# Kernel optimization log

Measured on AMD Instinct MI355X. Metric: run time of the kernel, lower is better.

Reference implementation:

```python
import jax, jax.numpy as jnp
import numpy as np
import math

B, S, D, H, NF = 2, 2048, 1024, 16, 4
DH = D // H


def setup_inputs() -> dict:
    key = jax.random.key(0)
    ks = jax.random.split(key, 8)
    scale = 0.01 / math.sqrt(D)  # rough attenuated-kaiming scale for projections
    return {
        "x": jax.random.normal(ks[0], (B, S, D), dtype=jnp.float32),
        "weights": jax.random.uniform(ks[1], (1, NF), dtype=jnp.float32),
        "Wq": jax.random.normal(ks[2], (D, D), dtype=jnp.float32) * scale,
        "bq": jnp.zeros((D,), dtype=jnp.float32),
        "Wk": jax.random.normal(ks[3], (D, D), dtype=jnp.float32) * scale,
        "bk": jnp.zeros((D,), dtype=jnp.float32),
        "Wv": jax.random.normal(ks[4], (D, D), dtype=jnp.float32) * scale,
        "bv": jnp.zeros((D,), dtype=jnp.float32),
        "Wout": jax.random.normal(ks[5], (NF, D, D), dtype=jnp.float32) / math.sqrt(D),
        "bout": jnp.zeros((NF, D), dtype=jnp.float32),
    }


def reference(x, weights, Wq, bq, Wk, bk, Wv, bv, Wout, bout):
    # projections (torch Linear: x @ W.T + b)
    q = x @ Wq.T + bq  # [B,S,D]
    k = x @ Wk.T + bk
    v = x @ Wv.T + bv
    # split heads -> [B,H,S,DH]
    split = lambda t: t.reshape(B, S, H, DH).transpose(0, 2, 1, 3)
    q, k, v = split(q), split(k), split(v)
    # scores with causal additive mask of -10000 (as in get_attention_mask)
    scores = jnp.einsum("bhqd,bhkd->bhqk", q, k) / math.sqrt(DH)
    i = jnp.arange(S)
    causal = (i[None, :] <= i[:, None])  # [S,S] True where allowed
    mask = (1.0 - causal.astype(scores.dtype)) * -10000.0
    attn = jax.nn.softmax(scores + mask, axis=-1)
    # dropout is disabled (p=0.0)
    out = jnp.einsum("bhqk,bhkd->bhqd", attn, v)  # [B,H,S,DH]
    out = out.transpose(0, 2, 1, 3).reshape(B, S, D)
    # WeightedFunctions: per-function Linear(d,d) combined by weights[0]
    w0 = weights[0]  # [NF]
    Weff = jnp.einsum("f,fod->od", w0, Wout)  # [D,D]
    beff = w0 @ bout  # [D]
    return out @ Weff.T + beff
```

## Files before the change

### kernel.cpp

```cpp
#include <hip/hip_runtime.h>


typedef unsigned short u16;
typedef __bf16 bf16_t;
typedef bf16_t bf16x8 __attribute__((ext_vector_type(8)));
typedef bf16_t bf16x4 __attribute__((ext_vector_type(4)));
typedef float f32x4 __attribute__((ext_vector_type(4)));
typedef u16 u16x8 __attribute__((ext_vector_type(8)));
typedef u16 u16x4 __attribute__((ext_vector_type(4)));

#define DEV __device__ __forceinline__

DEV u16 f2bf(float f) {
  unsigned u = __float_as_uint(f);
  u += 0x7FFFu + ((u >> 16) & 1u);
  return (u16)(u >> 16);
}

DEV void async_ld16(const void* g, void* lds_wave_uniform) {
  __builtin_amdgcn_global_load_lds(
      (const __attribute__((address_space(1))) void*)g,
      (__attribute__((address_space(3))) void*)lds_wave_uniform, 16, 0, 0);
}

__global__ __launch_bounds__(256) void cvt_bf16_kernel(
    const float* __restrict__ in, u16* __restrict__ out, int n4) {
  int i = blockIdx.x * blockDim.x + threadIdx.x;
  const int stride = gridDim.x * blockDim.x;
  for (; i < n4; i += stride) {
    const float4 v = ((const float4*)in)[i];
    u16x4 o;
    o[0] = f2bf(v.x); o[1] = f2bf(v.y); o[2] = f2bf(v.z); o[3] = f2bf(v.w);
    ((u16x4*)out)[i] = o;
  }
}

__global__ __launch_bounds__(256) void cvt3_bf16_kernel(
    const float* __restrict__ a, const float* __restrict__ b,
    const float* __restrict__ c, u16* __restrict__ out) {
  const int i = blockIdx.x * 256 + threadIdx.x;
  const int which = i >> 18;
  const int j = i & 262143;
  const float* src = which == 0 ? a : (which == 1 ? b : c);
  const float4 v = ((const float4*)src)[j];
  u16x4 o;
  o[0] = f2bf(v.x); o[1] = f2bf(v.y); o[2] = f2bf(v.z); o[3] = f2bf(v.w);
  ((u16x4*)out)[i] = o;
}

__global__ __launch_bounds__(256) void build_weff_kernel(
    const float* __restrict__ w4, const float* __restrict__ Wout,
    const float* __restrict__ bout, u16* __restrict__ Weff,
    float* __restrict__ beff) {
  constexpr int DD4 = 262144;
  const int i = blockIdx.x * blockDim.x + threadIdx.x;
  if (i >= DD4) return;
  const float w0 = w4[0], w1 = w4[1], w2 = w4[2], w3 = w4[3];
  const float4* W = (const float4*)Wout;
  const float4 a = W[i], b1 = W[DD4 + i], b2 = W[2 * DD4 + i], b3 = W[3 * DD4 + i];
  u16x4 o;
  o[0] = f2bf(w0 * a.x + w1 * b1.x + w2 * b2.x + w3 * b3.x);
  o[1] = f2bf(w0 * a.y + w1 * b1.y + w2 * b2.y + w3 * b3.y);
  o[2] = f2bf(w0 * a.z + w1 * b1.z + w2 * b2.z + w3 * b3.z);
  o[3] = f2bf(w0 * a.w + w1 * b1.w + w2 * b2.w + w3 * b3.w);
  ((u16x4*)Weff)[i] = o;
  if (i < 256) {
    const float4* B4 = (const float4*)bout;
    const float4 ba = B4[i], c1 = B4[256 + i], c2 = B4[512 + i], c3 = B4[768 + i];
    float4 ob;
    ob.x = w0 * ba.x + w1 * c1.x + w2 * c2.x + w3 * c3.x;
    ob.y = w0 * ba.y + w1 * c1.y + w2 * c2.y + w3 * c3.y;
    ob.z = w0 * ba.z + w1 * c1.z + w2 * c2.z + w3 * c3.z;
    ob.w = w0 * ba.w + w1 * c1.w + w2 * c2.w + w3 * c3.w;
    ((float4*)beff)[i] = ob;
  }
}

__global__ __launch_bounds__(256) void gemm_bt_kernel(
    const u16* __restrict__ A, const u16* __restrict__ Bw,
    const float* __restrict__ bias, float* __restrict__ C, int M, int N, int K) {
  constexpr int BM = 128, BK = 32;
  __shared__ u16 As[2][BM * BK];
  __shared__ u16 Bs[2][BM * BK];
  const int tid = threadIdx.x;
  const int w = tid >> 6, lane = tid & 63;
  const int l15 = lane & 15, l4 = lane >> 4;
  const int wr = w >> 1, wc = w & 1;
  const long m0 = (long)blockIdx.y * BM, n0 = (long)blockIdx.x * BM;

  const int sr = (tid * 16) >> 6;
  const int sc = ((tid * 16) & 63) >> 1;

  auto stage = [&](int buf, int kt) {
#pragma unroll
    for (int is = 0; is < 2; ++is) {
      const int r = sr + is * 64;
      async_ld16(A + (m0 + r) * K + kt + sc, &As[buf][w * 512 + is * 2048]);
      async_ld16(Bw + (n0 + r) * K + kt + sc, &Bs[buf][w * 512 + is * 2048]);
    }
  };

  f32x4 acc[4][4] = {};
  stage(0, 0);
  __syncthreads();
  const int nt = K / BK;
  for (int t = 0; t < nt; ++t) {
    const int buf = t & 1;
    if (t + 1 < nt) stage(buf ^ 1, (t + 1) * BK);
    bf16x8 af[4], bfrag[4];
#pragma unroll
    for (int i = 0; i < 4; ++i) {
      af[i] = *(const bf16x8*)&As[buf][(wr * 64 + i * 16 + l15) * BK + l4 * 8];
      bfrag[i] = *(const bf16x8*)&Bs[buf][(wc * 64 + i * 16 + l15) * BK + l4 * 8];
    }
#pragma unroll
    for (int i = 0; i < 4; ++i)
#pragma unroll
      for (int j = 0; j < 4; ++j)
        acc[i][j] = __builtin_amdgcn_mfma_f32_16x16x32_bf16(af[i], bfrag[j],
                                                            acc[i][j], 0, 0, 0);
    __syncthreads();
  }

#pragma unroll
  for (int i = 0; i < 4; ++i) {
    const long row0 = m0 + wr * 64 + i * 16 + l4 * 4;
#pragma unroll
    for (int j = 0; j < 4; ++j) {
      const long col = n0 + wc * 64 + j * 16 + l15;
      const float bb = bias[col];
#pragma unroll
      for (int r = 0; r < 4; ++r)
        C[(row0 + r) * N + col] = acc[i][j][r] + bb;
    }
  }
}

__global__ __launch_bounds__(256) void gemm_qkv_kernel(
    const u16* __restrict__ A, const u16* __restrict__ Bw,
    const float* __restrict__ bq, const float* __restrict__ bk,
    const float* __restrict__ bv, u16* __restrict__ qo, u16* __restrict__ ko,
    u16* __restrict__ vo) {
  constexpr int K = 1024, BK = 32;
  __shared__ u16 SM[16384];
  u16* As = SM;
  u16* Bs = SM + 8192;
  const int tid = threadIdx.x;
  const int w = tid >> 6, lane = tid & 63;
  const int l15 = lane & 15, l4 = lane >> 4;
  const int wr = w >> 1, wc = w & 1;
  const long m0 = (long)blockIdx.y * 128, n0 = (long)blockIdx.x * 128;
  const int seg = blockIdx.x >> 3;
  const float* bias = seg == 0 ? bq : (seg == 1 ? bk : bv);
  u16* outp = seg == 0 ? qo : (seg == 1 ? ko : vo);
  const float scale = seg == 0 ? 0.18033688011112042f : 1.0f;

  const int sr = (tid * 16) >> 6;
  const int sc = ((tid * 16) & 63) >> 1;

  auto stage = [&](int buf, int kt) {
#pragma unroll
    for (int is = 0; is < 2; ++is) {
      const int r = sr + is * 64;
      async_ld16(A + (m0 + r) * K + kt + sc, &As[buf * 4096 + w * 512 + is * 2048]);
      async_ld16(Bw + (n0 + r) * K + kt + sc, &Bs[buf * 4096 + w * 512 + is * 2048]);
    }
  };

  f32x4 acc[4][4] = {};
  stage(0, 0);
  __syncthreads();
  const int nt = K / BK;
  for (int t = 0; t < nt; ++t) {
    const int buf = t & 1;
    if (t + 1 < nt) stage(buf ^ 1, (t + 1) * BK);
    bf16x8 af[4], bfrag[4];
#pragma unroll
    for (int i = 0; i < 4; ++i) {
      af[i] = *(const bf16x8*)&As[buf * 4096 + (wr * 64 + i * 16 + l15) * BK + l4 * 8];
      bfrag[i] = *(const bf16x8*)&Bs[buf * 4096 + (wc * 64 + i * 16 + l15) * BK + l4 * 8];
    }
#pragma unroll
    for (int i = 0; i < 4; ++i)
#pragma unroll
      for (int j = 0; j < 4; ++j)
        acc[i][j] = __builtin_amdgcn_mfma_f32_16x16x32_bf16(af[i], bfrag[j],
                                                            acc[i][j], 0, 0, 0);
    __syncthreads();
  }

  const long ccol0 = n0 - (long)seg * 1024;
#pragma unroll
  for (int i = 0; i < 4; ++i) {
#pragma unroll
    for (int j = 0; j < 4; ++j) {
      const int colb = wc * 64 + j * 16 + l15;
      const float bb = bias[ccol0 + colb];
#pragma unroll
      for (int r = 0; r < 4; ++r) {
        const int row = wr * 64 + i * 16 + l4 * 4 + r;
        SM[row * 128 + (colb ^ ((row & 15) << 3))] =
            f2bf((acc[i][j][r] + bb) * scale);
      }
    }
  }
  __syncthreads();
#pragma unroll
  for (int p = 0; p < 8; ++p) {
    const int cid = p * 256 + tid;
    const int row = cid >> 4, c = cid & 15;
    const u16x8 vch = *(const u16x8*)&SM[row * 128 + ((c ^ (row & 15)) * 8)];
    *(u16x8*)&outp[(m0 + row) * 1024 + ccol0 + c * 8] = vch;
  }
}

__global__ __launch_bounds__(256) void transpose_v_kernel(
    const u16* __restrict__ V, u16* __restrict__ Vt) {
  constexpr int S = 2048, D = 1024, DH = 64;
  __shared__ u16 T[64 * 72];
  const int tid = threadIdx.x;
  const int bh = blockIdx.y, b = bh >> 4, h = bh & 15;
  const int s0 = blockIdx.x * 64;
#pragma unroll
  for (int is = 0; is < 2; ++is) {
    const int sl = tid + is * 256;
    const int r = sl >> 3, c0 = (sl & 7) * 8;
    *(u16x8*)&T[r * 72 + c0] =
        *(const u16x8*)(V + (size_t)(b * S + s0 + r) * D + h * DH + c0);
  }
  __syncthreads();
#pragma unroll
  for (int is = 0; is < 2; ++is) {
    const int sl = tid + is * 256;
    const int d = sl >> 3, k0 = (sl & 7) * 8;
    u16x8 o;
#pragma unroll
    for (int j = 0; j < 8; ++j) o[j] = T[(k0 + j) * 72 + d];
    *(u16x8*)(Vt + (size_t)(bh * DH + d) * S + s0 + k0) = o;
  }
}

__global__ __launch_bounds__(512, 6) void flash_kernel(
    const u16* __restrict__ Q, const u16* __restrict__ Kg,
    const u16* __restrict__ Vt, u16* __restrict__ O,
    u16* __restrict__ accP, float* __restrict__ mP, float* __restrict__ lP) {
  constexpr int S = 2048, D = 1024, DH = 64;
  __shared__ u16 Ks[2][4096];
  __shared__ u16 Vs[2][4096];
  __shared__ u16 Ps[8192];
  const int tid = threadIdx.x;
  const int w = tid >> 6, lane = tid & 63;
  const int l15 = lane & 15, l4 = lane >> 4;
  const int bh = blockIdx.y, b = bh >> 4, h = bh & 15;
  const int x = 23 - (int)blockIdx.x;
  int bi, kvlo, kvhi, seg;
  if (x < 8) {
    bi = x; seg = -1; kvlo = 0; kvhi = 2 * bi + 2;
  } else {
    const int idx = x - 8;
    bi = 8 + (idx >> 1); seg = idx & 1;
    kvlo = seg ? (bi + 1) : 0;
    kvhi = seg ? (2 * bi + 2) : (bi + 1);
  }
  const int qw = 128 * bi + w * 16;
  const int qtile = qw >> 6;

  const u16* Kbh = Kg + (size_t)b * S * D + h * DH;
  const u16* Vbh = Vt + (size_t)bh * DH * S;

  const int srow = tid >> 3;
  const int scol = ((tid & 7) ^ (srow & 7)) * 8;
  const int sw = l15 & 7;

  bf16x8 qf[2];
  {
    const u16* qp = Q + (size_t)(b * S + qw + l15) * D + h * DH + l4 * 8;
    qf[0] = *(const bf16x8*)qp;
    qf[1] = *(const bf16x8*)(qp + 32);
  }

  f32x4 acc_o[4] = {};
  float m_run = -3e38f, l_run = 0.f;

  async_ld16(Kbh + (size_t)(kvlo * 64 + srow) * D + scol, &Ks[0][w * 512]);
  async_ld16(Vbh + (size_t)srow * S + kvlo * 64 + scol, &Vs[0][w * 512]);
  __syncthreads();

  for (int it = kvlo; it < kvhi; ++it) {
    const int buf = (it - kvlo) & 1;
    if (it + 1 < kvhi) {
      async_ld16(Kbh + (size_t)((it + 1) * 64 + srow) * D + scol,
                 &Ks[buf ^ 1][w * 512]);
      async_ld16(Vbh + (size_t)srow * S + (it + 1) * 64 + scol,
                 &Vs[buf ^ 1][w * 512]);
    }
    if (it <= qtile) {
      f32x4 accs[4] = {};
#pragma unroll
      for (int cb = 0; cb < 4; ++cb) {
        const int row = cb * 16 + l15;
        const bf16x8 kf0 = *(const bf16x8*)&Ks[buf][row * 64 + ((l4 ^ sw) * 8)];
        const bf16x8 kf1 =
            *(const bf16x8*)&Ks[buf][row * 64 + (((l4 + 4) ^ sw) * 8)];
        accs[cb] =
            __builtin_amdgcn_mfma_f32_16x16x32_bf16(kf0, qf[0], accs[cb], 0, 0, 0);
        accs[cb] =
            __builtin_amdgcn_mfma_f32_16x16x32_bf16(kf1, qf[1], accs[cb], 0, 0, 0);
      }
      float mx = -3e38f;
      if (it == qtile) {
#pragma unroll
        for (int cb = 0; cb < 4; ++cb)
#pragma unroll
          for (int r = 0; r < 4; ++r) {
            float s_ = accs[cb][r];
            if (it * 64 + cb * 16 + l4 * 4 + r > qw + l15) s_ = -3e38f;
            accs[cb][r] = s_;
            mx = fmaxf(mx, s_);
          }
      } else {
#pragma unroll
        for (int cb = 0; cb < 4; ++cb)
#pragma unroll
          for (int r = 0; r < 4; ++r) mx = fmaxf(mx, accs[cb][r]);
      }
      mx = fmaxf(mx, __shfl_xor(mx, 16));
      mx = fmaxf(mx, __shfl_xor(mx, 32));
      if (!__all(mx - m_run <= 8.0f)) {
        const float mn = fmaxf(m_run, mx);
        const float corr = __builtin_amdgcn_exp2f(m_run - mn);
        m_run = mn;
        float cq[4];
#pragma unroll
        for (int r = 0; r < 4; ++r) cq[r] = __shfl(corr, l4 * 4 + r, 64);
#pragma unroll
        for (int db = 0; db < 4; ++db)
#pragma unroll
          for (int r = 0; r < 4; ++r) acc_o[db][r] *= cq[r];
        l_run *= corr;
      }
      float rs = 0.f;
#pragma unroll
      for (int cb = 0; cb < 4; ++cb)
#pragma unroll
        for (int r = 0; r < 4; ++r) {
          const float pv = __builtin_amdgcn_exp2f(accs[cb][r] - m_run);
          accs[cb][r] = pv;
          rs += pv;
        }
      rs += __shfl_xor(rs, 16);
      rs += __shfl_xor(rs, 32);
      l_run += rs;
#pragma unroll
      for (int cb = 0; cb < 4; ++cb) {
        bf16x4 pk = {(bf16_t)accs[cb][0], (bf16_t)accs[cb][1],
                     (bf16_t)accs[cb][2], (bf16_t)accs[cb][3]};
        const int chunk = (2 * cb + (l4 >> 1)) ^ sw;
        *(bf16x4*)&Ps[w * 1024 + l15 * 64 + chunk * 8 + (l4 & 1) * 4] = pk;
      }
      asm volatile("s_waitcnt lgkmcnt(0)" ::: "memory");
      bf16x8 pa[2];
#pragma unroll
      for (int mf = 0; mf < 2; ++mf) {
        const int chunk = (mf * 4 + l4) ^ sw;
        pa[mf] = *(const bf16x8*)&Ps[w * 1024 + l15 * 64 + chunk * 8];
      }
#pragma unroll
      for (int db = 0; db < 4; ++db) {
        const int row = db * 16 + l15;
        const bf16x8 vf0 = *(const bf16x8*)&Vs[buf][row * 64 + ((l4 ^ sw) * 8)];
        const bf16x8 vf1 =
            *(const bf16x8*)&Vs[buf][row * 64 + (((l4 + 4) ^ sw) * 8)];
        acc_o[db] =
            __builtin_amdgcn_mfma_f32_16x16x32_bf16(pa[0], vf0, acc_o[db], 0, 0, 0);
        acc_o[db] =
            __builtin_amdgcn_mfma_f32_16x16x32_bf16(pa[1], vf1, acc_o[db], 0, 0, 0);
      }
    }
    __syncthreads();
  }

  float lq[4];
  if (seg < 0) {
#pragma unroll
    for (int r = 0; r < 4; ++r) lq[r] = __shfl(l_run, l4 * 4 + r, 64);
  }
#pragma unroll
  for (int db = 0; db < 4; ++db) {
#pragma unroll
    for (int r = 0; r < 4; ++r) {
      const int row = l4 * 4 + r;
      const int col = db * 16 + l15;
      const float v = seg < 0 ? acc_o[db][r] / lq[r] : acc_o[db][r];
      Ps[w * 1024 + row * 64 + (col ^ ((row & 7) << 3))] = f2bf(v);
    }
  }
  asm volatile("s_waitcnt lgkmcnt(0)" ::: "memory");
  if (seg < 0) {
#pragma unroll
    for (int j = 0; j < 2; ++j) {
      const int cid = j * 64 + lane;
      const int row = cid >> 3, c = cid & 7;
      const u16x8 vch =
          *(const u16x8*)&Ps[w * 1024 + row * 64 + ((c ^ (row & 7)) * 8)];
      *(u16x8*)&O[(size_t)(b * S + qw + row) * D + h * DH + c * 8] = vch;
    }
  } else {
    const size_t base = (size_t)seg * 32768 + (size_t)bh * 1024 + (qw - 1024);
#pragma unroll
    for (int j = 0; j < 2; ++j) {
      const int cid = j * 64 + lane;
      const int row = cid >> 3, c = cid & 7;
      const u16x8 vch =
          *(const u16x8*)&Ps[w * 1024 + row * 64 + ((c ^ (row & 7)) * 8)];
      *(u16x8*)&accP[(base + row) * 64 + c * 8] = vch;
    }
    if (l4 == 0) {
      mP[base + l15] = m_run;
      lP[base + l15] = l_run;
    }
  }
}

__global__ __launch_bounds__(256) void combine_kernel(
    const u16* __restrict__ accP, const float* __restrict__ mP,
    const float* __restrict__ lP, u16* __restrict__ O) {
  const int id = blockIdx.x * 256 + threadIdx.x;
  const int row = id >> 3;
  const int c0 = (id & 7) * 8;
  const float m0 = mP[row], m1 = mP[32768 + row];
  const float l0 = lP[row], l1 = lP[32768 + row];
  const float M = fmaxf(m0, m1);
  const float e0 = __builtin_amdgcn_exp2f(m0 - M);
  const float e1 = __builtin_amdgcn_exp2f(m1 - M);
  const float inv = 1.f / (l0 * e0 + l1 * e1);
  const bf16_t* aP = (const bf16_t*)accP;
  const bf16x8 a0 = *(const bf16x8*)&aP[(size_t)row * 64 + c0];
  const bf16x8 a1 = *(const bf16x8*)&aP[(size_t)(32768 + row) * 64 + c0];
  const int bh = row >> 10, s = 1024 + (row & 1023);
  const int b = bh >> 4, h = bh & 15;
  bf16_t* out = (bf16_t*)O + (size_t)(b * 2048 + s) * 1024 + h * 64 + c0;
  bf16x8 o;
#pragma unroll
  for (int j = 0; j < 8; ++j)
    o[j] = (bf16_t)(((float)a0[j] * e0 + (float)a1[j] * e1) * inv);
  *(bf16x8*)out = o;
}

extern "C" void kernel_launch(void* const* d_in, const int* in_sizes, int n_in,
                              void* d_out, int out_size, void* d_ws, size_t ws_size,
                              hipStream_t stream) {
  (void)in_sizes; (void)n_in; (void)out_size;
  const float* x   = (const float*)d_in[0];
  const float* wts = (const float*)d_in[1];
  const float* Wq  = (const float*)d_in[2];
  const float* bq  = (const float*)d_in[3];
  const float* Wk  = (const float*)d_in[4];
  const float* bk  = (const float*)d_in[5];
  const float* Wv  = (const float*)d_in[6];
  const float* bv  = (const float*)d_in[7];
  const float* Wo  = (const float*)d_in[8];
  const float* bo  = (const float*)d_in[9];
  float* out = (float*)d_out;

  if (ws_size < 58724352) return;

  char* ws = (char*)d_ws;
  u16* xbf  = (u16*)(ws + 0);
  u16* qbf  = (u16*)(ws + 8388608);
  u16* kbf  = (u16*)(ws + 16777216);
  u16* vbf  = (u16*)(ws + 25165824);
  u16* vt   = (u16*)(ws + 33554432);
  u16* attn = (u16*)(ws + 41943040);
  u16* wqkv = (u16*)(ws + 50331648);
  u16* wob  = (u16*)(ws + 56623104);
  float* beff = (float*)(ws + 58720256);

  u16* accP = xbf;
  float* mP = (float*)(ws + 50331648);
  float* lP = mP + 65536;

  cvt_bf16_kernel<<<2048, 256, 0, stream>>>(x, xbf, 1048576);
  cvt3_bf16_kernel<<<3072, 256, 0, stream>>>(Wq, Wk, Wv, wqkv);
  build_weff_kernel<<<1024, 256, 0, stream>>>(wts, Wo, bo, wob, beff);

  gemm_qkv_kernel<<<dim3(24, 32), 256, 0, stream>>>(xbf, wqkv, bq, bk, bv,
                                                    qbf, kbf, vbf);
  transpose_v_kernel<<<dim3(32, 32), 256, 0, stream>>>(vbf, vt);
  flash_kernel<<<dim3(24, 32), 512, 0, stream>>>(qbf, kbf, vt, attn,
                                                 accP, mP, lP);
  combine_kernel<<<1024, 256, 0, stream>>>(accP, mP, lP, attn);
  gemm_bt_kernel<<<dim3(8, 32), 256, 0, stream>>>(
      attn, wob, beff, out, 4096, 1024, 1024);
}
```

Before: 126.7 us.

## Fuse prep kernels, widen GEMM K-tile with swizzle, fuse V transpose, defer row reductions

Merges the three conversion and weight-combine kernels into one grid-stride prep kernel. Both GEMMs now use a 64-wide K tile with an XOR-swizzled LDS layout and two MFMAs per fragment pair. The QKV GEMM writes V already transposed through LDS, which removes the separate transpose kernel and the round trip of V through global memory. In the flash kernel, the cross-lane max and sum shuffles are skipped on the fast path, and the row-sum reduction happens once at the end. The cost is larger LDS use per block, which may reduce occupancy.

```diff
diff --git a/kernel.cpp b/kernel.cpp
--- a/kernel.cpp
+++ b/kernel.cpp
@@ -23,102 +23,113 @@
       (__attribute__((address_space(3))) void*)lds_wave_uniform, 16, 0, 0);
 }
 
-__global__ __launch_bounds__(256) void cvt_bf16_kernel(
-    const float* __restrict__ in, u16* __restrict__ out, int n4) {
-  int i = blockIdx.x * blockDim.x + threadIdx.x;
-  const int stride = gridDim.x * blockDim.x;
-  for (; i < n4; i += stride) {
-    const float4 v = ((const float4*)in)[i];
-    u16x4 o;
-    o[0] = f2bf(v.x); o[1] = f2bf(v.y); o[2] = f2bf(v.z); o[3] = f2bf(v.w);
-    ((u16x4*)out)[i] = o;
-  }
-}
-
-__global__ __launch_bounds__(256) void cvt3_bf16_kernel(
-    const float* __restrict__ a, const float* __restrict__ b,
-    const float* __restrict__ c, u16* __restrict__ out) {
-  const int i = blockIdx.x * 256 + threadIdx.x;
-  const int which = i >> 18;
-  const int j = i & 262143;
-  const float* src = which == 0 ? a : (which == 1 ? b : c);
-  const float4 v = ((const float4*)src)[j];
-  u16x4 o;
-  o[0] = f2bf(v.x); o[1] = f2bf(v.y); o[2] = f2bf(v.z); o[3] = f2bf(v.w);
-  ((u16x4*)out)[i] = o;
-}
-
-__global__ __launch_bounds__(256) void build_weff_kernel(
+__global__ __launch_bounds__(256) void prep_kernel(
+    const float* __restrict__ x, const float* __restrict__ Wq,
+    const float* __restrict__ Wk, const float* __restrict__ Wv,
     const float* __restrict__ w4, const float* __restrict__ Wout,
-    const float* __restrict__ bout, u16* __restrict__ Weff,
-    float* __restrict__ beff) {
-  constexpr int DD4 = 262144;
-  const int i = blockIdx.x * blockDim.x + threadIdx.x;
-  if (i >= DD4) return;
-  const float w0 = w4[0], w1 = w4[1], w2 = w4[2], w3 = w4[3];
-  const float4* W = (const float4*)Wout;
-  const float4 a = W[i], b1 = W[DD4 + i], b2 = W[2 * DD4 + i], b3 = W[3 * DD4 + i];
-  u16x4 o;
-  o[0] = f2bf(w0 * a.x + w1 * b1.x + w2 * b2.x + w3 * b3.x);
-  o[1] = f2bf(w0 * a.y + w1 * b1.y + w2 * b2.y + w3 * b3.y);
-  o[2] = f2bf(w0 * a.z + w1 * b1.z + w2 * b2.z + w3 * b3.z);
-  o[3] = f2bf(w0 * a.w + w1 * b1.w + w2 * b2.w + w3 * b3.w);
-  ((u16x4*)Weff)[i] = o;
-  if (i < 256) {
-    const float4* B4 = (const float4*)bout;
-    const float4 ba = B4[i], c1 = B4[256 + i], c2 = B4[512 + i], c3 = B4[768 + i];
-    float4 ob;
-    ob.x = w0 * ba.x + w1 * c1.x + w2 * c2.x + w3 * c3.x;
-    ob.y = w0 * ba.y + w1 * c1.y + w2 * c2.y + w3 * c3.y;
-    ob.z = w0 * ba.z + w1 * c1.z + w2 * c2.z + w3 * c3.z;
-    ob.w = w0 * ba.w + w1 * c1.w + w2 * c2.w + w3 * c3.w;
-    ((float4*)beff)[i] = ob;
-  }
-}
+    const float* __restrict__ bout, u16* __restrict__ xbf,
+    u16* __restrict__ wqkv, u16* __restrict__ Weff, float* __restrict__ beff) {
+  constexpr int NX = 1048576;
+  constexpr int NW = 262144;
+  const int stride = gridDim.x * 256;
+  for (int id = blockIdx.x * 256 + threadIdx.x; id < NX + 3 * NW + NW;
+       id += stride) {
+    if (id < NX) {
+      const float4 v = ((const float4*)x)[id];
+      u16x4 o;
+      o[0] = f2bf(v.x); o[1] = f2bf(v.y); o[2] = f2bf(v.z); o[3] = f2bf(v.w);
+      ((u16x4*)xbf)[id] = o;
+    } else if (id < NX + 3 * NW) {
+      const int wi = id - NX;
+      const int which = wi >> 18, j = wi & (NW - 1);
+      const float* src = which == 0 ? Wq : (which == 1 ? Wk : Wv);
+      const float4 v = ((const float4*)src)[j];
+      u16x4 o;
+      o[0] = f2bf(v.x); o[1] = f2bf(v.y); o[2] = f2bf(v.z); o[3] = f2bf(v.w);
+      ((u16x4*)wqkv)[wi] = o;
+    } else {
+      const int i = id - NX - 3 * NW;
+      const float w0 = w4[0], w1 = w4[1], w2 = w4[2], w3 = w4[3];
+      const float4* W = (const float4*)Wout;
+      const float4 a = W[i], b1 = W[NW + i], b2 = W[2 * NW + i],
+                   b3 = W[3 * NW + i];
+      u16x4 o;
+      o[0] = f2bf(w0 * a.x + w1 * b1.x + w2 * b2.x + w3 * b3.x);
+      o[1] = f2bf(w0 * a.y + w1 * b1.y + w2 * b2.y + w3 * b3.y);
+      o[2] = f2bf(w0 * a.z + w1 * b1.z + w2 * b2.z + w3 * b3.z);
+      o[3] = f2bf(w0 * a.w + w1 * b1.w + w2 * b2.w + w3 * b3.w);
+      ((u16x4*)Weff)[i] = o;
+      if (i < 256) {
+        const float4* B4 = (const float4*)bout;
+        const float4 ba = B4[i], c1 = B4[256 + i], c2 = B4[512 + i],
+                     c3 = B4[768 + i];
+        float4 ob;
+        ob.x = w0 * ba.x + w1 * c1.x + w2 * c2.x + w3 * c3.x;
+        ob.y = w0 * ba.y + w1 * c1.y + w2 * c2.y + w3 * c3.y;
+        ob.z = w0 * ba.z + w1 * c1.z + w2 * c2.z + w3 * c3.z;
+        ob.w = w0 * ba.w + w1 * c1.w + w2 * c2.w + w3 * c3.w;
+        ((float4*)beff)[i] = ob;
+      }
+    }
+  }
+}
+
 
 __global__ __launch_bounds__(256) void gemm_bt_kernel(
     const u16* __restrict__ A, const u16* __restrict__ Bw,
     const float* __restrict__ bias, float* __restrict__ C, int M, int N, int K) {
-  constexpr int BM = 128, BK = 32;
-  __shared__ u16 As[2][BM * BK];
-  __shared__ u16 Bs[2][BM * BK];
+  __shared__ u16 LDS[32768];
   const int tid = threadIdx.x;
   const int w = tid >> 6, lane = tid & 63;
   const int l15 = lane & 15, l4 = lane >> 4;
   const int wr = w >> 1, wc = w & 1;
-  const long m0 = (long)blockIdx.y * BM, n0 = (long)blockIdx.x * BM;
-
-  const int sr = (tid * 16) >> 6;
-  const int sc = ((tid * 16) & 63) >> 1;
-
+  const long m0 = (long)blockIdx.y * 128, n0 = (long)blockIdx.x * 128;
+
+  int srow[4], scol[4];
+#pragma unroll
+  for (int d = 0; d < 4; ++d) {
+    srow[d] = d * 32 + w * 8 + (lane >> 3);
+    scol[d] = ((lane & 7) ^ (srow[d] & 7)) * 8;
+  }
   auto stage = [&](int buf, int kt) {
 #pragma unroll
-    for (int is = 0; is < 2; ++is) {
-      const int r = sr + is * 64;
-      async_ld16(A + (m0 + r) * K + kt + sc, &As[buf][w * 512 + is * 2048]);
-      async_ld16(Bw + (n0 + r) * K + kt + sc, &Bs[buf][w * 512 + is * 2048]);
+    for (int d = 0; d < 4; ++d) {
+      async_ld16(A + (m0 + srow[d]) * K + kt + scol[d],
+                 &LDS[buf * 8192 + d * 2048 + w * 512]);
+      async_ld16(Bw + (n0 + srow[d]) * K + kt + scol[d],
+                 &LDS[16384 + buf * 8192 + d * 2048 + w * 512]);
     }
   };
 
   f32x4 acc[4][4] = {};
   stage(0, 0);
   __syncthreads();
-  const int nt = K / BK;
+  const int nt = K / 64;
   for (int t = 0; t < nt; ++t) {
     const int buf = t & 1;
-    if (t + 1 < nt) stage(buf ^ 1, (t + 1) * BK);
-    bf16x8 af[4], bfrag[4];
+    if (t + 1 < nt) stage(buf ^ 1, (t + 1) * 64);
+    bf16x8 af[4][2], bf[4][2];
 #pragma unroll
     for (int i = 0; i < 4; ++i) {
-      af[i] = *(const bf16x8*)&As[buf][(wr * 64 + i * 16 + l15) * BK + l4 * 8];
-      bfrag[i] = *(const bf16x8*)&Bs[buf][(wc * 64 + i * 16 + l15) * BK + l4 * 8];
+      const int ra = wr * 64 + i * 16 + l15;
+      const int rb = wc * 64 + i * 16 + l15;
+#pragma unroll
+      for (int ks = 0; ks < 2; ++ks) {
+        af[i][ks] = *(const bf16x8*)&LDS[buf * 8192 + ra * 64 +
+                                         (((ks * 4 + l4) ^ (ra & 7)) * 8)];
+        bf[i][ks] = *(const bf16x8*)&LDS[16384 + buf * 8192 + rb * 64 +
+                                         (((ks * 4 + l4) ^ (rb & 7)) * 8)];
+      }
     }
 #pragma unroll
     for (int i = 0; i < 4; ++i)
 #pragma unroll
-      for (int j = 0; j < 4; ++j)
-        acc[i][j] = __builtin_amdgcn_mfma_f32_16x16x32_bf16(af[i], bfrag[j],
+      for (int j = 0; j < 4; ++j) {
+        acc[i][j] = __builtin_amdgcn_mfma_f32_16x16x32_bf16(af[i][0], bf[j][0],
                                                             acc[i][j], 0, 0, 0);
+        acc[i][j] = __builtin_amdgcn_mfma_f32_16x16x32_bf16(af[i][1], bf[j][1],
+                                                            acc[i][j], 0, 0, 0);
+      }
     __syncthreads();
   }
 
@@ -140,11 +151,9 @@
     const u16* __restrict__ A, const u16* __restrict__ Bw,
     const float* __restrict__ bq, const float* __restrict__ bk,
     const float* __restrict__ bv, u16* __restrict__ qo, u16* __restrict__ ko,
-    u16* __restrict__ vo) {
-  constexpr int K = 1024, BK = 32;
-  __shared__ u16 SM[16384];
-  u16* As = SM;
-  u16* Bs = SM + 8192;
+    u16* __restrict__ vt) {
+  constexpr int K = 1024;
+  __shared__ u16 LDS[32768];
   const int tid = threadIdx.x;
   const int w = tid >> 6, lane = tid & 63;
   const int l15 = lane & 15, l4 = lane >> 4;
@@ -152,91 +161,107 @@
   const long m0 = (long)blockIdx.y * 128, n0 = (long)blockIdx.x * 128;
   const int seg = blockIdx.x >> 3;
   const float* bias = seg == 0 ? bq : (seg == 1 ? bk : bv);
-  u16* outp = seg == 0 ? qo : (seg == 1 ? ko : vo);
   const float scale = seg == 0 ? 0.18033688011112042f : 1.0f;
 
-  const int sr = (tid * 16) >> 6;
-  const int sc = ((tid * 16) & 63) >> 1;
-
+  int srow[4], scol[4];
+#pragma unroll
+  for (int d = 0; d < 4; ++d) {
+    srow[d] = d * 32 + w * 8 + (lane >> 3);
+    scol[d] = ((lane & 7) ^ (srow[d] & 7)) * 8;
+  }
   auto stage = [&](int buf, int kt) {
 #pragma unroll
-    for (int is = 0; is < 2; ++is) {
-      const int r = sr + is * 64;
-      async_ld16(A + (m0 + r) * K + kt + sc, &As[buf * 4096 + w * 512 + is * 2048]);
-      async_ld16(Bw + (n0 + r) * K + kt + sc, &Bs[buf * 4096 + w * 512 + is * 2048]);
+    for (int d = 0; d < 4; ++d) {
+      async_ld16(A + (m0 + srow[d]) * K + kt + scol[d],
+                 &LDS[buf * 8192 + d * 2048 + w * 512]);
+      async_ld16(Bw + (n0 + srow[d]) * K + kt + scol[d],
+                 &LDS[16384 + buf * 8192 + d * 2048 + w * 512]);
     }
   };
 
   f32x4 acc[4][4] = {};
   stage(0, 0);
   __syncthreads();
-  const int nt = K / BK;
+  const int nt = K / 64;
   for (int t = 0; t < nt; ++t) {
     const int buf = t & 1;
-    if (t + 1 < nt) stage(buf ^ 1, (t + 1) * BK);
-    bf16x8 af[4], bfrag[4];
+    if (t + 1 < nt) stage(buf ^ 1, (t + 1) * 64);
+    bf16x8 af[4][2], bf[4][2];
 #pragma unroll
     for (int i = 0; i < 4; ++i) {
-      af[i] = *(const bf16x8*)&As[buf * 4096 + (wr * 64 + i * 16 + l15) * BK + l4 * 8];
-      bfrag[i] = *(const bf16x8*)&Bs[buf * 4096 + (wc * 64 + i * 16 + l15) * BK + l4 * 8];
+      const int ra = wr * 64 + i * 16 + l15;
+      const int rb = wc * 64 + i * 16 + l15;
+#pragma unroll
+      for (int ks = 0; ks < 2; ++ks) {
+        af[i][ks] = *(const bf16x8*)&LDS[buf * 8192 + ra * 64 +
+                                         (((ks * 4 + l4) ^ (ra & 7)) * 8)];
+        bf[i][ks] = *(const bf16x8*)&LDS[16384 + buf * 8192 + rb * 64 +
+                                         (((ks * 4 + l4) ^ (rb & 7)) * 8)];
+      }
     }
 #pragma unroll
     for (int i = 0; i < 4; ++i)
 #pragma unroll
-      for (int j = 0; j < 4; ++j)
-        acc[i][j] = __builtin_amdgcn_mfma_f32_16x16x32_bf16(af[i], bfrag[j],
+      for (int j = 0; j < 4; ++j) {
+        acc[i][j] = __builtin_amdgcn_mfma_f32_16x16x32_bf16(af[i][0], bf[j][0],
                                                             acc[i][j], 0, 0, 0);
+        acc[i][j] = __builtin_amdgcn_mfma_f32_16x16x32_bf16(af[i][1], bf[j][1],
+                                                            acc[i][j], 0, 0, 0);
+      }
     __syncthreads();
   }
 
   const long ccol0 = n0 - (long)seg * 1024;
-#pragma unroll
-  for (int i = 0; i < 4; ++i) {
-#pragma unroll
-    for (int j = 0; j < 4; ++j) {
-      const int colb = wc * 64 + j * 16 + l15;
-      const float bb = bias[ccol0 + colb];
-#pragma unroll
-      for (int r = 0; r < 4; ++r) {
-        const int row = wr * 64 + i * 16 + l4 * 4 + r;
-        SM[row * 128 + (colb ^ ((row & 15) << 3))] =
-            f2bf((acc[i][j][r] + bb) * scale);
-      }
-    }
-  }
-  __syncthreads();
-#pragma unroll
-  for (int p = 0; p < 8; ++p) {
-    const int cid = p * 256 + tid;
-    const int row = cid >> 4, c = cid & 15;
-    const u16x8 vch = *(const u16x8*)&SM[row * 128 + ((c ^ (row & 15)) * 8)];
-    *(u16x8*)&outp[(m0 + row) * 1024 + ccol0 + c * 8] = vch;
-  }
-}
-
-__global__ __launch_bounds__(256) void transpose_v_kernel(
-    const u16* __restrict__ V, u16* __restrict__ Vt) {
-  constexpr int S = 2048, D = 1024, DH = 64;
-  __shared__ u16 T[64 * 72];
-  const int tid = threadIdx.x;
-  const int bh = blockIdx.y, b = bh >> 4, h = bh & 15;
-  const int s0 = blockIdx.x * 64;
-#pragma unroll
-  for (int is = 0; is < 2; ++is) {
-    const int sl = tid + is * 256;
-    const int r = sl >> 3, c0 = (sl & 7) * 8;
-    *(u16x8*)&T[r * 72 + c0] =
-        *(const u16x8*)(V + (size_t)(b * S + s0 + r) * D + h * DH + c0);
-  }
-  __syncthreads();
-#pragma unroll
-  for (int is = 0; is < 2; ++is) {
-    const int sl = tid + is * 256;
-    const int d = sl >> 3, k0 = (sl & 7) * 8;
-    u16x8 o;
-#pragma unroll
-    for (int j = 0; j < 8; ++j) o[j] = T[(k0 + j) * 72 + d];
-    *(u16x8*)(Vt + (size_t)(bh * DH + d) * S + s0 + k0) = o;
+  if (seg < 2) {
+    u16* outp = seg == 0 ? qo : ko;
+#pragma unroll
+    for (int i = 0; i < 4; ++i) {
+#pragma unroll
+      for (int j = 0; j < 4; ++j) {
+        const int colb = wc * 64 + j * 16 + l15;
+        const float bb = bias[ccol0 + colb];
+#pragma unroll
+        for (int r = 0; r < 4; ++r) {
+          const int row = wr * 64 + i * 16 + l4 * 4 + r;
+          LDS[row * 128 + (colb ^ ((row & 15) << 3))] =
+              f2bf((acc[i][j][r] + bb) * scale);
+        }
+      }
+    }
+    __syncthreads();
+#pragma unroll
+    for (int p = 0; p < 8; ++p) {
+      const int cid = p * 256 + tid;
+      const int row = cid >> 4, c = cid & 15;
+      const u16x8 vch = *(const u16x8*)&LDS[row * 128 + ((c ^ (row & 15)) * 8)];
+      *(u16x8*)&outp[(m0 + row) * 1024 + ccol0 + c * 8] = vch;
+    }
+  } else {
+    const int b = (int)(m0 >> 11);
+    const int s0 = (int)(m0 & 2047);
+#pragma unroll
+    for (int i = 0; i < 4; ++i) {
+#pragma unroll
+      for (int j = 0; j < 4; ++j) {
+        const int colb = wc * 64 + j * 16 + l15;
+        const float bb = bias[ccol0 + colb];
+#pragma unroll
+        for (int r = 0; r < 4; ++r) {
+          const int row = wr * 64 + i * 16 + l4 * 4 + r;
+          LDS[colb * 128 + (row ^ ((colb & 15) << 3))] = f2bf(acc[i][j][r] + bb);
+        }
+      }
+    }
+    __syncthreads();
+#pragma unroll
+    for (int p = 0; p < 8; ++p) {
+      const int cid = p * 256 + tid;
+      const int c = cid >> 4, r0 = (cid & 15) * 8;
+      const u16x8 vch = *(const u16x8*)&LDS[c * 128 + (r0 ^ ((c & 15) << 3))];
+      const int gcol = (int)ccol0 + c;
+      const int h = gcol >> 6, d = gcol & 63;
+      *(u16x8*)&vt[(size_t)((b * 16 + h) * 64 + d) * 2048 + s0 + r0] = vch;
+    }
   }
 }
 
@@ -324,9 +349,9 @@
 #pragma unroll
           for (int r = 0; r < 4; ++r) mx = fmaxf(mx, accs[cb][r]);
       }
-      mx = fmaxf(mx, __shfl_xor(mx, 16));
-      mx = fmaxf(mx, __shfl_xor(mx, 32));
       if (!__all(mx - m_run <= 8.0f)) {
+        mx = fmaxf(mx, __shfl_xor(mx, 16));
+        mx = fmaxf(mx, __shfl_xor(mx, 32));
         const float mn = fmaxf(m_run, mx);
         const float corr = __builtin_amdgcn_exp2f(m_run - mn);
         m_run = mn;
@@ -348,8 +373,6 @@
           accs[cb][r] = pv;
           rs += pv;
         }
-      rs += __shfl_xor(rs, 16);
-      rs += __shfl_xor(rs, 32);
       l_run += rs;
 #pragma unroll
       for (int cb = 0; cb < 4; ++cb) {
@@ -380,10 +403,13 @@
     __syncthreads();
   }
 
+  float l_tot = l_run;
+  l_tot += __shfl_xor(l_tot, 16);
+  l_tot += __shfl_xor(l_tot, 32);
   float lq[4];
   if (seg < 0) {
 #pragma unroll
-    for (int r = 0; r < 4; ++r) lq[r] = __shfl(l_run, l4 * 4 + r, 64);
+    for (int r = 0; r < 4; ++r) lq[r] = __shfl(l_tot, l4 * 4 + r, 64);
   }
 #pragma unroll
   for (int db = 0; db < 4; ++db) {
@@ -417,7 +443,7 @@
     }
     if (l4 == 0) {
       mP[base + l15] = m_run;
-      lP[base + l15] = l_run;
+      lP[base + l15] = l_tot;
     }
   }
 }
@@ -469,7 +495,6 @@
   u16* xbf  = (u16*)(ws + 0);
   u16* qbf  = (u16*)(ws + 8388608);
   u16* kbf  = (u16*)(ws + 16777216);
-  u16* vbf  = (u16*)(ws + 25165824);
   u16* vt   = (u16*)(ws + 33554432);
   u16* attn = (u16*)(ws + 41943040);
   u16* wqkv = (u16*)(ws + 50331648);
@@ -480,13 +505,10 @@
   float* mP = (float*)(ws + 50331648);
   float* lP = mP + 65536;
 
-  cvt_bf16_kernel<<<2048, 256, 0, stream>>>(x, xbf, 1048576);
-  cvt3_bf16_kernel<<<3072, 256, 0, stream>>>(Wq, Wk, Wv, wqkv);
-  build_weff_kernel<<<1024, 256, 0, stream>>>(wts, Wo, bo, wob, beff);
-
+  prep_kernel<<<2048, 256, 0, stream>>>(x, Wq, Wk, Wv, wts, Wo, bo,
+                                        xbf, wqkv, wob, beff);
   gemm_qkv_kernel<<<dim3(24, 32), 256, 0, stream>>>(xbf, wqkv, bq, bk, bv,
-                                                    qbf, kbf, vbf);
-  transpose_v_kernel<<<dim3(32, 32), 256, 0, stream>>>(vbf, vt);
+                                                    qbf, kbf, vt);
   flash_kernel<<<dim3(24, 32), 512, 0, stream>>>(qbf, kbf, vt, attn,
                                                  accP, mP, lP);
   combine_kernel<<<1024, 256, 0, stream>>>(accP, mP, lP, attn);
```

Result: faster. 108.2 us (-14.6%).
